# Optimization experiments

Hardware: AMD Instinct MI355X
Metric: run time of the kernel (lower is better)

## Reference

```python
import jax, jax.numpy as jnp
import numpy as np

HIDDEN = 256
HEADS = 8
HEAD_DIM = HIDDEN // HEADS
NUM_RBF = 32
CUTOFF = 8.0
K_PTS = 4096   # total points (32 molecules x 128)
N_ATOMS = 2048 # total atoms  (32 molecules x 64)
B_MOL = 32


def setup_inputs() -> dict:
    key = jax.random.key(0)
    ks = jax.random.split(key, 12)
    s = 0.02
    return {
        "h_point": jax.random.normal(ks[0], (K_PTS, HIDDEN), jnp.float32),
        "h_atom": jax.random.normal(ks[1], (N_ATOMS, HIDDEN), jnp.float32),
        "pos_point": jax.random.uniform(ks[2], (K_PTS, 3), jnp.float32) * 10.0,
        "pos_atom": jax.random.uniform(ks[3], (N_ATOMS, 3), jnp.float32) * 10.0,
        "Wq": jax.random.normal(ks[4], (HIDDEN, HIDDEN), jnp.float32) * s,
        "bq": jnp.zeros((HIDDEN,), jnp.float32),
        "Wk": jax.random.normal(ks[5], (HIDDEN, HIDDEN), jnp.float32) * s,
        "bk": jnp.zeros((HIDDEN,), jnp.float32),
        "Wv": jax.random.normal(ks[6], (HIDDEN, HIDDEN), jnp.float32) * s,
        "bv": jnp.zeros((HIDDEN,), jnp.float32),
        "Wo": jax.random.normal(ks[7], (HIDDEN, HIDDEN), jnp.float32) * s,
        "bo": jnp.zeros((HIDDEN,), jnp.float32),
        "W_rbf": jax.random.normal(ks[8], (NUM_RBF, HEADS), jnp.float32) * 0.1,
        "b_rbf": jnp.zeros((HEADS,), jnp.float32),
        "centers": jnp.linspace(0.0, CUTOFF, NUM_RBF, dtype=jnp.float32),
        "gamma": jnp.ones((HIDDEN,), jnp.float32),
        "beta": jnp.zeros((HIDDEN,), jnp.float32),
        "point_batch": jnp.repeat(jnp.arange(B_MOL), K_PTS // B_MOL),
        "atom_batch": jnp.repeat(jnp.arange(B_MOL), N_ATOMS // B_MOL),
    }


def reference(h_point, h_atom, pos_point, pos_atom,
              Wq, bq, Wk, bk, Wv, bv, Wo, bo,
              W_rbf, b_rbf, centers, gamma, beta,
              point_batch, atom_batch):
    H, D = HEADS, HEAD_DIM
    Kp = h_point.shape[0]
    Na = h_atom.shape[0]
    scale = D ** -0.5
    width = (CUTOFF / NUM_RBF) ** 2

    q = (h_point @ Wq + bq).reshape(Kp, H, D)
    k = (h_atom @ Wk + bk).reshape(Na, H, D)
    v = (h_atom @ Wv + bv).reshape(Na, H, D)

    # pairwise distances [Kp, Na]
    d2 = jnp.sum((pos_point[:, None, :] - pos_atom[None, :, :]) ** 2, axis=-1)
    dist = jnp.sqrt(jnp.maximum(d2, 0.0))

    # RBF distance bias -> [H, Kp, Na]
    rbf = jnp.exp(-((dist[..., None] - centers) ** 2) / width)  # [Kp, Na, NUM_RBF]
    bias = (rbf @ W_rbf + b_rbf).transpose(2, 0, 1)

    scores = jnp.einsum('khd,nhd->hkn', q, k) * scale + bias
    # ragged structure: point j only attends to atoms in the same molecule
    mask = point_batch[:, None] == atom_batch[None, :]  # [Kp, Na]
    scores = jnp.where(mask[None], scores, -1e30)
    attn = jax.nn.softmax(scores, axis=-1)

    agg = jnp.einsum('hkn,nhd->khd', attn, v).reshape(Kp, H * D)
    agg = agg @ Wo + bo

    x = h_point + agg
    mean = jnp.mean(x, axis=-1, keepdims=True)
    var = jnp.mean((x - mean) ** 2, axis=-1, keepdims=True)
    return (x - mean) * jax.lax.rsqrt(var + 1e-5) * gamma + beta
```

## Files before the change

kernel.cpp:

```cpp
#include <hip/hip_runtime.h>
#include <hip/hip_bf16.h>

#define HIDDEN 256
#define HEADS 8
#define HEAD_DIM 32
#define NUM_RBF 32
#define K_PTS 4096
#define N_ATOMS 2048
#define B_MOL 32
#define ATOMS_PER_MOL (N_ATOMS / B_MOL)

typedef __attribute__((ext_vector_type(8))) short bf16x8;
typedef __attribute__((ext_vector_type(4))) float f32x4;

__global__ __launch_bounds__(256) void prep2_kernel(
    const float* __restrict__ hp, const float* __restrict__ ha,
    const float* __restrict__ Wq, const float* __restrict__ Wk,
    const float* __restrict__ Wv, const float* __restrict__ Wo,
    __hip_bfloat16* __restrict__ hpb, __hip_bfloat16* __restrict__ hab,
    __hip_bfloat16* __restrict__ WqT, __hip_bfloat16* __restrict__ WkT,
    __hip_bfloat16* __restrict__ WvT, __hip_bfloat16* __restrict__ WoT) {
    const int b = blockIdx.x, tid = threadIdx.x;
    if (b < 768) {
        const bool isP = (b < 512);
        const float* __restrict__ src = isP ? hp : ha;
        __hip_bfloat16* __restrict__ dst = isP ? hpb : hab;
        const int e8 = ((isP ? b : b - 512) * 256 + tid);
        const float4* s4 = (const float4*)src;
        const float4 lo = s4[e8 * 2 + 0];
        const float4 hi = s4[e8 * 2 + 1];
        __hip_bfloat16 t[8];
        t[0] = __float2bfloat16(lo.x); t[1] = __float2bfloat16(lo.y);
        t[2] = __float2bfloat16(lo.z); t[3] = __float2bfloat16(lo.w);
        t[4] = __float2bfloat16(hi.x); t[5] = __float2bfloat16(hi.y);
        t[6] = __float2bfloat16(hi.z); t[7] = __float2bfloat16(hi.w);
        *(uint4*)(dst + (size_t)e8 * 8) = *(const uint4*)t;
        return;
    }
    __shared__ float tile[32][33];
    const int t = b - 768;
    const int matId = t >> 6, tileId = t & 63;
    const int tr = (tileId >> 3) * 32, tc = (tileId & 7) * 32;
    const float* __restrict__ Ws = (matId == 0) ? Wq : (matId == 1) ? Wk : (matId == 2) ? Wv : Wo;
    __hip_bfloat16* __restrict__ Wd = (matId == 0) ? WqT : (matId == 1) ? WkT : (matId == 2) ? WvT : WoT;

    const int r = tid >> 3, cq = (tid & 7) * 4;
    const float4 in = *(const float4*)&Ws[(size_t)(tr + r) * HIDDEN + tc + cq];
    tile[r][cq + 0] = in.x; tile[r][cq + 1] = in.y;
    tile[r][cq + 2] = in.z; tile[r][cq + 3] = in.w;
    __syncthreads();
    __hip_bfloat16 o[4];
    o[0] = __float2bfloat16(tile[cq + 0][r]);
    o[1] = __float2bfloat16(tile[cq + 1][r]);
    o[2] = __float2bfloat16(tile[cq + 2][r]);
    o[3] = __float2bfloat16(tile[cq + 3][r]);
    *(uint2*)(Wd + (size_t)(tc + r) * HIDDEN + tr + cq) = *(const uint2*)o;
}

__global__ __launch_bounds__(256) void qkv_kernel(
    const __hip_bfloat16* __restrict__ hpb, const __hip_bfloat16* __restrict__ hab,
    const __hip_bfloat16* __restrict__ WqT, const float* __restrict__ bq, float* __restrict__ q_ws,
    const __hip_bfloat16* __restrict__ WkT, const float* __restrict__ bk, float* __restrict__ k_ws,
    const __hip_bfloat16* __restrict__ WvT, const float* __restrict__ bv, float* __restrict__ v_ws) {
    const bool isQ = (blockIdx.x < 256);
    const __hip_bfloat16* __restrict__ A = isQ ? hpb : hab;
    const __hip_bfloat16* __restrict__ W0T = isQ ? WqT : WkT;
    const float* __restrict__ b0 = isQ ? bq : bk;
    float* __restrict__ C0 = isQ ? q_ws : k_ws;
    const int r0 = (isQ ? blockIdx.x : blockIdx.x - 256) * 16;

    const int wave = threadIdx.x >> 6, lane = threadIdx.x & 63;
    const int c0 = wave * 64;
    const int lrow = lane & 15, kgrp = lane >> 4;

    bf16x8 af[8];
    const short* Arow = (const short*)A + (size_t)(r0 + lrow) * HIDDEN + kgrp * 8;
#pragma unroll
    for (int ks = 0; ks < 8; ++ks)
        af[ks] = *(const bf16x8*)(Arow + ks * 32);

    f32x4 acc0[4], acc1[4];
#pragma unroll
    for (int cc = 0; cc < 4; ++cc) {
        acc0[cc] = (f32x4){0.f, 0.f, 0.f, 0.f};
        acc1[cc] = (f32x4){0.f, 0.f, 0.f, 0.f};
    }

#pragma unroll
    for (int cc = 0; cc < 4; ++cc) {
        const short* W0r = (const short*)W0T + (size_t)(c0 + cc * 16 + lrow) * HIDDEN + kgrp * 8;
#pragma unroll
        for (int ks = 0; ks < 8; ++ks)
            acc0[cc] = __builtin_amdgcn_mfma_f32_16x16x32_bf16(
                af[ks], *(const bf16x8*)(W0r + ks * 32), acc0[cc], 0, 0, 0);
        if (!isQ) {
            const short* W1r = (const short*)WvT + (size_t)(c0 + cc * 16 + lrow) * HIDDEN + kgrp * 8;
#pragma unroll
            for (int ks = 0; ks < 8; ++ks)
                acc1[cc] = __builtin_amdgcn_mfma_f32_16x16x32_bf16(
                    af[ks], *(const bf16x8*)(W1r + ks * 32), acc1[cc], 0, 0, 0);
        }
    }

    const int colb = lane & 15;
    const int rowb = (lane >> 4) * 4;
#pragma unroll
    for (int cc = 0; cc < 4; ++cc) {
        const int cgl = c0 + cc * 16 + colb;
        const float bias0 = b0[cgl];
#pragma unroll
        for (int rg = 0; rg < 4; ++rg)
            C0[(size_t)(r0 + rowb + rg) * HIDDEN + cgl] = acc0[cc][rg] + bias0;
        if (!isQ) {
            const float bias1 = bv[cgl];
#pragma unroll
            for (int rg = 0; rg < 4; ++rg)
                v_ws[(size_t)(r0 + rowb + rg) * HIDDEN + cgl] = acc1[cc][rg] + bias1;
        }
    }
}

__global__ __launch_bounds__(256) void attn3_kernel(
    const float* __restrict__ q, const float* __restrict__ kmat,
    const float* __restrict__ vmat,
    const float* __restrict__ pos_point, const float* __restrict__ pos_atom,
    const float* __restrict__ W_rbf, const float* __restrict__ b_rbf,
    const float* __restrict__ centers,
    const int* __restrict__ point_batch, const int* __restrict__ atom_batch,
    __hip_bfloat16* __restrict__ aggb) {
    __shared__ float q_lds[8][HIDDEN];
    __shared__ float wrbf_lds[NUM_RBF][HEADS];
    __shared__ float cent_lds[NUM_RBF];
    __shared__ float brbf_lds[HEADS];
    __shared__ float w_lds[4][2][HEADS][72];

    const int tid = threadIdx.x, wave = tid >> 6, lane = tid & 63;
    const int j0 = blockIdx.x * 8;

    {
        const float4* s4 = (const float4*)(q + (size_t)j0 * HIDDEN);
        float4* d4 = (float4*)&q_lds[0][0];
        d4[tid] = s4[tid];
        d4[tid + 256] = s4[tid + 256];
    }
    if (tid < NUM_RBF * HEADS) ((float*)wrbf_lds)[tid] = W_rbf[tid];
    if (tid < NUM_RBF) cent_lds[tid] = centers[tid];
    if (tid < HEADS) brbf_lds[tid] = b_rbf[tid];
    __syncthreads();

    const int jA = j0 + wave * 2, jB = jA + 1;
    const int m = point_batch[jA];
    const int n = m * ATOMS_PER_MOL + lane;
    const bool valid = (atom_batch[n] == m);

    const float ax = pos_atom[n * 3 + 0], ay = pos_atom[n * 3 + 1], az = pos_atom[n * 3 + 2];
    const float dxA = pos_point[jA * 3 + 0] - ax;
    const float dyA = pos_point[jA * 3 + 1] - ay;
    const float dzA = pos_point[jA * 3 + 2] - az;
    const float dxB = pos_point[jB * 3 + 0] - ax;
    const float dyB = pos_point[jB * 3 + 1] - ay;
    const float dzB = pos_point[jB * 3 + 2] - az;
    const float distA = sqrtf(fmaxf(dxA * dxA + dyA * dyA + dzA * dzA, 0.0f));
    const float distB = sqrtf(fmaxf(dxB * dxB + dyB * dyB + dzB * dzB, 0.0f));

    float biasA[HEADS], biasB[HEADS];
#pragma unroll
    for (int h = 0; h < HEADS; ++h) { biasA[h] = brbf_lds[h]; biasB[h] = brbf_lds[h]; }
#pragma unroll
    for (int r = 0; r < NUM_RBF; ++r) {
        const float c = cent_lds[r];
        const float ddA = distA - c, ddB = distB - c;
        const float eA = __expf(-16.0f * ddA * ddA);
        const float eB = __expf(-16.0f * ddB * ddB);
#pragma unroll
        for (int h = 0; h < HEADS; ++h) {
            const float wr = wrbf_lds[r][h];
            biasA[h] += eA * wr;
            biasB[h] += eB * wr;
        }
    }

    const float scale = 0.17677669529663687f;
    const float* krow = kmat + (size_t)n * HIDDEN;

#pragma unroll
    for (int h = 0; h < HEADS; ++h) {
        const float4* k4 = (const float4*)(krow + h * HEAD_DIM);
        const float4* qA4 = (const float4*)(&q_lds[wave * 2 + 0][h * HEAD_DIM]);
        const float4* qB4 = (const float4*)(&q_lds[wave * 2 + 1][h * HEAD_DIM]);
        float dotA = 0.f, dotB = 0.f;
#pragma unroll
        for (int i = 0; i < HEAD_DIM / 4; ++i) {
            const float4 kv = k4[i];
            const float4 qa = qA4[i];
            const float4 qb = qB4[i];
            dotA += kv.x * qa.x + kv.y * qa.y + kv.z * qa.z + kv.w * qa.w;
            dotB += kv.x * qb.x + kv.y * qb.y + kv.z * qb.z + kv.w * qb.w;
        }
        float sA = valid ? (dotA * scale + biasA[h]) : -1e30f;
        float sB = valid ? (dotB * scale + biasB[h]) : -1e30f;

        float mA = sA, mB = sB;
#pragma unroll
        for (int off = 32; off > 0; off >>= 1) {
            mA = fmaxf(mA, __shfl_xor(mA, off));
            mB = fmaxf(mB, __shfl_xor(mB, off));
        }
        const float eA = __expf(sA - mA);
        const float eB = __expf(sB - mB);
        float ssA = eA, ssB = eB;
#pragma unroll
        for (int off = 32; off > 0; off >>= 1) {
            ssA += __shfl_xor(ssA, off);
            ssB += __shfl_xor(ssB, off);
        }
        w_lds[wave][0][h][lane] = eA / ssA;
        w_lds[wave][1][h][lane] = eB / ssB;
    }

    const int c4 = lane * 4;
    const int hh = lane >> 3;
    const float* wA = &w_lds[wave][0][hh][0];
    const float* wB = &w_lds[wave][1][hh][0];
    const float* vbase = vmat + (size_t)(m * ATOMS_PER_MOL) * HIDDEN + c4;
    float4 accA = {0.f, 0.f, 0.f, 0.f};
    float4 accB = {0.f, 0.f, 0.f, 0.f};
#pragma unroll
    for (int a4 = 0; a4 < ATOMS_PER_MOL / 4; ++a4) {
        const float4 wa = *(const float4*)&wA[a4 * 4];
        const float4 wb = *(const float4*)&wB[a4 * 4];
        const float4 v0 = *(const float4*)(vbase + (size_t)(a4 * 4 + 0) * HIDDEN);
        const float4 v1 = *(const float4*)(vbase + (size_t)(a4 * 4 + 1) * HIDDEN);
        const float4 v2 = *(const float4*)(vbase + (size_t)(a4 * 4 + 2) * HIDDEN);
        const float4 v3 = *(const float4*)(vbase + (size_t)(a4 * 4 + 3) * HIDDEN);
        accA.x += wa.x * v0.x + wa.y * v1.x + wa.z * v2.x + wa.w * v3.x;
        accA.y += wa.x * v0.y + wa.y * v1.y + wa.z * v2.y + wa.w * v3.y;
        accA.z += wa.x * v0.z + wa.y * v1.z + wa.z * v2.z + wa.w * v3.z;
        accA.w += wa.x * v0.w + wa.y * v1.w + wa.z * v2.w + wa.w * v3.w;
        accB.x += wb.x * v0.x + wb.y * v1.x + wb.z * v2.x + wb.w * v3.x;
        accB.y += wb.x * v0.y + wb.y * v1.y + wb.z * v2.y + wb.w * v3.y;
        accB.z += wb.x * v0.z + wb.y * v1.z + wb.z * v2.z + wb.w * v3.z;
        accB.w += wb.x * v0.w + wb.y * v1.w + wb.z * v2.w + wb.w * v3.w;
    }
    {
        __hip_bfloat16 oA[4], oB[4];
        oA[0] = __float2bfloat16(accA.x); oA[1] = __float2bfloat16(accA.y);
        oA[2] = __float2bfloat16(accA.z); oA[3] = __float2bfloat16(accA.w);
        oB[0] = __float2bfloat16(accB.x); oB[1] = __float2bfloat16(accB.y);
        oB[2] = __float2bfloat16(accB.z); oB[3] = __float2bfloat16(accB.w);
        *(uint2*)(aggb + (size_t)jA * HIDDEN + c4) = *(const uint2*)oA;
        *(uint2*)(aggb + (size_t)jB * HIDDEN + c4) = *(const uint2*)oB;
    }
}

__global__ __launch_bounds__(256) void gemm_o_ln_kernel(
    const __hip_bfloat16* __restrict__ A,
    const __hip_bfloat16* __restrict__ WoT, const float* __restrict__ bo,
    const float* __restrict__ h_point,
    const float* __restrict__ gamma, const float* __restrict__ beta,
    float* __restrict__ out) {
    __shared__ float x_lds[16][HIDDEN + 1];
    __shared__ float red_s[16][4];
    __shared__ float red_q[16][4];

    const int r0 = blockIdx.x * 16;
    const int wave = threadIdx.x >> 6, lane = threadIdx.x & 63;
    const int c0 = wave * 64;
    const int lrow = lane & 15, kgrp = lane >> 4;

    bf16x8 af[8];
    const short* Arow = (const short*)A + (size_t)(r0 + lrow) * HIDDEN + kgrp * 8;
#pragma unroll
    for (int ks = 0; ks < 8; ++ks)
        af[ks] = *(const bf16x8*)(Arow + ks * 32);

    f32x4 acc[4];
#pragma unroll
    for (int cc = 0; cc < 4; ++cc) acc[cc] = (f32x4){0.f, 0.f, 0.f, 0.f};

#pragma unroll
    for (int cc = 0; cc < 4; ++cc) {
        const short* Wr = (const short*)WoT + (size_t)(c0 + cc * 16 + lrow) * HIDDEN + kgrp * 8;
#pragma unroll
        for (int ks = 0; ks < 8; ++ks)
            acc[cc] = __builtin_amdgcn_mfma_f32_16x16x32_bf16(
                af[ks], *(const bf16x8*)(Wr + ks * 32), acc[cc], 0, 0, 0);
    }

    const int colb = lane & 15;
    const int rowb = (lane >> 4) * 4;
#pragma unroll
    for (int cc = 0; cc < 4; ++cc) {
        const int cgl = c0 + cc * 16 + colb;
        const float bias = bo[cgl];
#pragma unroll
        for (int rg = 0; rg < 4; ++rg) {
            const int rl = rowb + rg;
            x_lds[rl][cgl] = acc[cc][rg] + bias + h_point[(size_t)(r0 + rl) * HIDDEN + cgl];
        }
    }
    __syncthreads();

    const int c = threadIdx.x;
    const int ln = c & 63, wv = c >> 6;
    float xv[16];
#pragma unroll
    for (int r = 0; r < 16; ++r) {
        xv[r] = x_lds[r][c];
        float s = xv[r], qq = xv[r] * xv[r];
#pragma unroll
        for (int off = 32; off > 0; off >>= 1) {
            s += __shfl_xor(s, off);
            qq += __shfl_xor(qq, off);
        }
        if (ln == 0) { red_s[r][wv] = s; red_q[r][wv] = qq; }
    }
    __syncthreads();

    const float gc = gamma[c], bc = beta[c];
#pragma unroll
    for (int r = 0; r < 16; ++r) {
        const float mean = (red_s[r][0] + red_s[r][1] + red_s[r][2] + red_s[r][3]) * (1.0f / HIDDEN);
        const float ex2  = (red_q[r][0] + red_q[r][1] + red_q[r][2] + red_q[r][3]) * (1.0f / HIDDEN);
        const float var = ex2 - mean * mean;
        out[(size_t)(r0 + r) * HIDDEN + c] = (xv[r] - mean) * rsqrtf(var + 1e-5f) * gc + bc;
    }
}

extern "C" void kernel_launch(void* const* d_in, const int* in_sizes, int n_in,
                              void* d_out, int out_size, void* d_ws, size_t ws_size,
                              hipStream_t stream) {
    const float* h_point   = (const float*)d_in[0];
    const float* h_atom    = (const float*)d_in[1];
    const float* pos_point = (const float*)d_in[2];
    const float* pos_atom  = (const float*)d_in[3];
    const float* Wq        = (const float*)d_in[4];
    const float* bq        = (const float*)d_in[5];
    const float* Wk        = (const float*)d_in[6];
    const float* bk        = (const float*)d_in[7];
    const float* Wv        = (const float*)d_in[8];
    const float* bv        = (const float*)d_in[9];
    const float* Wo        = (const float*)d_in[10];
    const float* bo        = (const float*)d_in[11];
    const float* W_rbf     = (const float*)d_in[12];
    const float* b_rbf     = (const float*)d_in[13];
    const float* centers   = (const float*)d_in[14];
    const float* gamma     = (const float*)d_in[15];
    const float* beta      = (const float*)d_in[16];
    const int*   point_batch = (const int*)d_in[17];
    const int*   atom_batch  = (const int*)d_in[18];
    float* out = (float*)d_out;

    float* q_ws = (float*)d_ws;
    float* k_ws = q_ws + (size_t)K_PTS * HIDDEN;
    float* v_ws = k_ws + (size_t)N_ATOMS * HIDDEN;
    __hip_bfloat16* hp_b = (__hip_bfloat16*)(v_ws + (size_t)N_ATOMS * HIDDEN);
    __hip_bfloat16* ha_b = hp_b + (size_t)K_PTS * HIDDEN;
    __hip_bfloat16* WqT = ha_b + (size_t)N_ATOMS * HIDDEN;
    __hip_bfloat16* WkT = WqT + HIDDEN * HIDDEN;
    __hip_bfloat16* WvT = WkT + HIDDEN * HIDDEN;
    __hip_bfloat16* WoT = WvT + HIDDEN * HIDDEN;
    __hip_bfloat16* agg_b = hp_b;

    prep2_kernel<<<1024, 256, 0, stream>>>(h_point, h_atom, Wq, Wk, Wv, Wo,
                                           hp_b, ha_b, WqT, WkT, WvT, WoT);

    qkv_kernel<<<384, 256, 0, stream>>>(hp_b, ha_b,
                                        WqT, bq, q_ws,
                                        WkT, bk, k_ws,
                                        WvT, bv, v_ws);

    attn3_kernel<<<K_PTS / 8, 256, 0, stream>>>(q_ws, k_ws, v_ws, pos_point, pos_atom,
                                                W_rbf, b_rbf, centers,
                                                point_batch, atom_batch, agg_b);

    gemm_o_ln_kernel<<<K_PTS / 16, 256, 0, stream>>>(agg_b, WoT, bo, h_point,
                                                     gamma, beta, out);
}
```

Before: 147.1 us.

## Fuse activation bf16 conversion into QKV GEMM and O-proj+LayerNorm into attention

The bf16 conversion of h_point/h_atom moves out of the prep kernel and into the QKV GEMM's A-fragment loads, which removes one round trip of the activations through global memory. The output projection and LayerNorm are fused into the attention kernel: the aggregated rows stay in LDS as bf16 and feed MFMA directly, so the separate gemm_o_ln launch and the agg round trip go away. The cost is that the fused GEMM now handles 8 rows per block, padded to 16, so half the MFMA rows do wasted work, and each block reloads the WoT matrix.

```diff
diff --git a/kernel.cpp b/kernel.cpp
--- a/kernel.cpp
+++ b/kernel.cpp
@@ -13,32 +13,13 @@
 typedef __attribute__((ext_vector_type(8))) short bf16x8;
 typedef __attribute__((ext_vector_type(4))) float f32x4;
 
-__global__ __launch_bounds__(256) void prep2_kernel(
-    const float* __restrict__ hp, const float* __restrict__ ha,
+__global__ __launch_bounds__(256) void prepW_kernel(
     const float* __restrict__ Wq, const float* __restrict__ Wk,
     const float* __restrict__ Wv, const float* __restrict__ Wo,
-    __hip_bfloat16* __restrict__ hpb, __hip_bfloat16* __restrict__ hab,
     __hip_bfloat16* __restrict__ WqT, __hip_bfloat16* __restrict__ WkT,
     __hip_bfloat16* __restrict__ WvT, __hip_bfloat16* __restrict__ WoT) {
-    const int b = blockIdx.x, tid = threadIdx.x;
-    if (b < 768) {
-        const bool isP = (b < 512);
-        const float* __restrict__ src = isP ? hp : ha;
-        __hip_bfloat16* __restrict__ dst = isP ? hpb : hab;
-        const int e8 = ((isP ? b : b - 512) * 256 + tid);
-        const float4* s4 = (const float4*)src;
-        const float4 lo = s4[e8 * 2 + 0];
-        const float4 hi = s4[e8 * 2 + 1];
-        __hip_bfloat16 t[8];
-        t[0] = __float2bfloat16(lo.x); t[1] = __float2bfloat16(lo.y);
-        t[2] = __float2bfloat16(lo.z); t[3] = __float2bfloat16(lo.w);
-        t[4] = __float2bfloat16(hi.x); t[5] = __float2bfloat16(hi.y);
-        t[6] = __float2bfloat16(hi.z); t[7] = __float2bfloat16(hi.w);
-        *(uint4*)(dst + (size_t)e8 * 8) = *(const uint4*)t;
-        return;
-    }
     __shared__ float tile[32][33];
-    const int t = b - 768;
+    const int t = blockIdx.x, tid = threadIdx.x;
     const int matId = t >> 6, tileId = t & 63;
     const int tr = (tileId >> 3) * 32, tc = (tileId & 7) * 32;
     const float* __restrict__ Ws = (matId == 0) ? Wq : (matId == 1) ? Wk : (matId == 2) ? Wv : Wo;
@@ -57,13 +38,24 @@
     *(uint2*)(Wd + (size_t)(tc + r) * HIDDEN + tr + cq) = *(const uint2*)o;
 }
 
-__global__ __launch_bounds__(256) void qkv_kernel(
-    const __hip_bfloat16* __restrict__ hpb, const __hip_bfloat16* __restrict__ hab,
+__device__ __forceinline__ bf16x8 cvt8(const float* p) {
+    const float4 lo = *(const float4*)p;
+    const float4 hi = *(const float4*)(p + 4);
+    __hip_bfloat16 t[8];
+    t[0] = __float2bfloat16(lo.x); t[1] = __float2bfloat16(lo.y);
+    t[2] = __float2bfloat16(lo.z); t[3] = __float2bfloat16(lo.w);
+    t[4] = __float2bfloat16(hi.x); t[5] = __float2bfloat16(hi.y);
+    t[6] = __float2bfloat16(hi.z); t[7] = __float2bfloat16(hi.w);
+    return *(const bf16x8*)t;
+}
+
+__global__ __launch_bounds__(256) void qkv2_kernel(
+    const float* __restrict__ hp, const float* __restrict__ ha,
     const __hip_bfloat16* __restrict__ WqT, const float* __restrict__ bq, float* __restrict__ q_ws,
     const __hip_bfloat16* __restrict__ WkT, const float* __restrict__ bk, float* __restrict__ k_ws,
     const __hip_bfloat16* __restrict__ WvT, const float* __restrict__ bv, float* __restrict__ v_ws) {
     const bool isQ = (blockIdx.x < 256);
-    const __hip_bfloat16* __restrict__ A = isQ ? hpb : hab;
+    const float* __restrict__ A = isQ ? hp : ha;
     const __hip_bfloat16* __restrict__ W0T = isQ ? WqT : WkT;
     const float* __restrict__ b0 = isQ ? bq : bk;
     float* __restrict__ C0 = isQ ? q_ws : k_ws;
@@ -74,10 +66,10 @@
     const int lrow = lane & 15, kgrp = lane >> 4;
 
     bf16x8 af[8];
-    const short* Arow = (const short*)A + (size_t)(r0 + lrow) * HIDDEN + kgrp * 8;
+    const float* Arow = A + (size_t)(r0 + lrow) * HIDDEN + kgrp * 8;
 #pragma unroll
     for (int ks = 0; ks < 8; ++ks)
-        af[ks] = *(const bf16x8*)(Arow + ks * 32);
+        af[ks] = cvt8(Arow + ks * 32);
 
     f32x4 acc0[4], acc1[4];
 #pragma unroll
@@ -120,19 +112,29 @@
     }
 }
 
-__global__ __launch_bounds__(256) void attn3_kernel(
+#define AGG_PAD (HIDDEN + 16)
+#define X_PAD (HIDDEN + 4)
+
+__global__ __launch_bounds__(256) void attn_oln_kernel(
     const float* __restrict__ q, const float* __restrict__ kmat,
     const float* __restrict__ vmat,
     const float* __restrict__ pos_point, const float* __restrict__ pos_atom,
     const float* __restrict__ W_rbf, const float* __restrict__ b_rbf,
     const float* __restrict__ centers,
     const int* __restrict__ point_batch, const int* __restrict__ atom_batch,
-    __hip_bfloat16* __restrict__ aggb) {
+    const __hip_bfloat16* __restrict__ WoT, const float* __restrict__ bo,
+    const float* __restrict__ h_point,
+    const float* __restrict__ gamma, const float* __restrict__ beta,
+    float* __restrict__ out) {
     __shared__ float q_lds[8][HIDDEN];
     __shared__ float wrbf_lds[NUM_RBF][HEADS];
     __shared__ float cent_lds[NUM_RBF];
     __shared__ float brbf_lds[HEADS];
     __shared__ float w_lds[4][2][HEADS][72];
+    __shared__ __hip_bfloat16 agg_lds[8][AGG_PAD];
+    __shared__ float x_lds[8][X_PAD];
+    __shared__ float red_s[8][4];
+    __shared__ float red_q[8][4];
 
     const int tid = threadIdx.x, wave = tid >> 6, lane = tid & 63;
     const int j0 = blockIdx.x * 8;
@@ -220,64 +222,50 @@
 
     const int c4 = lane * 4;
     const int hh = lane >> 3;
-    const float* wA = &w_lds[wave][0][hh][0];
-    const float* wB = &w_lds[wave][1][hh][0];
-    const float* vbase = vmat + (size_t)(m * ATOMS_PER_MOL) * HIDDEN + c4;
-    float4 accA = {0.f, 0.f, 0.f, 0.f};
-    float4 accB = {0.f, 0.f, 0.f, 0.f};
-#pragma unroll
-    for (int a4 = 0; a4 < ATOMS_PER_MOL / 4; ++a4) {
-        const float4 wa = *(const float4*)&wA[a4 * 4];
-        const float4 wb = *(const float4*)&wB[a4 * 4];
-        const float4 v0 = *(const float4*)(vbase + (size_t)(a4 * 4 + 0) * HIDDEN);
-        const float4 v1 = *(const float4*)(vbase + (size_t)(a4 * 4 + 1) * HIDDEN);
-        const float4 v2 = *(const float4*)(vbase + (size_t)(a4 * 4 + 2) * HIDDEN);
-        const float4 v3 = *(const float4*)(vbase + (size_t)(a4 * 4 + 3) * HIDDEN);
-        accA.x += wa.x * v0.x + wa.y * v1.x + wa.z * v2.x + wa.w * v3.x;
-        accA.y += wa.x * v0.y + wa.y * v1.y + wa.z * v2.y + wa.w * v3.y;
-        accA.z += wa.x * v0.z + wa.y * v1.z + wa.z * v2.z + wa.w * v3.z;
-        accA.w += wa.x * v0.w + wa.y * v1.w + wa.z * v2.w + wa.w * v3.w;
-        accB.x += wb.x * v0.x + wb.y * v1.x + wb.z * v2.x + wb.w * v3.x;
-        accB.y += wb.x * v0.y + wb.y * v1.y + wb.z * v2.y + wb.w * v3.y;
-        accB.z += wb.x * v0.z + wb.y * v1.z + wb.z * v2.z + wb.w * v3.z;
-        accB.w += wb.x * v0.w + wb.y * v1.w + wb.z * v2.w + wb.w * v3.w;
-    }
     {
+        const float* wA = &w_lds[wave][0][hh][0];
+        const float* wB = &w_lds[wave][1][hh][0];
+        const float* vbase = vmat + (size_t)(m * ATOMS_PER_MOL) * HIDDEN + c4;
+        float4 accA = {0.f, 0.f, 0.f, 0.f};
+        float4 accB = {0.f, 0.f, 0.f, 0.f};
+#pragma unroll
+        for (int a4 = 0; a4 < ATOMS_PER_MOL / 4; ++a4) {
+            const float4 wa = *(const float4*)&wA[a4 * 4];
+            const float4 wb = *(const float4*)&wB[a4 * 4];
+            const float4 v0 = *(const float4*)(vbase + (size_t)(a4 * 4 + 0) * HIDDEN);
+            const float4 v1 = *(const float4*)(vbase + (size_t)(a4 * 4 + 1) * HIDDEN);
+            const float4 v2 = *(const float4*)(vbase + (size_t)(a4 * 4 + 2) * HIDDEN);
+            const float4 v3 = *(const float4*)(vbase + (size_t)(a4 * 4 + 3) * HIDDEN);
+            accA.x += wa.x * v0.x + wa.y * v1.x + wa.z * v2.x + wa.w * v3.x;
+            accA.y += wa.x * v0.y + wa.y * v1.y + wa.z * v2.y + wa.w * v3.y;
+            accA.z += wa.x * v0.z + wa.y * v1.z + wa.z * v2.z + wa.w * v3.z;
+            accA.w += wa.x * v0.w + wa.y * v1.w + wa.z * v2.w + wa.w * v3.w;
+            accB.x += wb.x * v0.x + wb.y * v1.x + wb.z * v2.x + wb.w * v3.x;
+            accB.y += wb.x * v0.y + wb.y * v1.y + wb.z * v2.y + wb.w * v3.y;
+            accB.z += wb.x * v0.z + wb.y * v1.z + wb.z * v2.z + wb.w * v3.z;
+            accB.w += wb.x * v0.w + wb.y * v1.w + wb.z * v2.w + wb.w * v3.w;
+        }
         __hip_bfloat16 oA[4], oB[4];
         oA[0] = __float2bfloat16(accA.x); oA[1] = __float2bfloat16(accA.y);
         oA[2] = __float2bfloat16(accA.z); oA[3] = __float2bfloat16(accA.w);
         oB[0] = __float2bfloat16(accB.x); oB[1] = __float2bfloat16(accB.y);
         oB[2] = __float2bfloat16(accB.z); oB[3] = __float2bfloat16(accB.w);
-        *(uint2*)(aggb + (size_t)jA * HIDDEN + c4) = *(const uint2*)oA;
-        *(uint2*)(aggb + (size_t)jB * HIDDEN + c4) = *(const uint2*)oB;
-    }
-}
-
-__global__ __launch_bounds__(256) void gemm_o_ln_kernel(
-    const __hip_bfloat16* __restrict__ A,
-    const __hip_bfloat16* __restrict__ WoT, const float* __restrict__ bo,
-    const float* __restrict__ h_point,
-    const float* __restrict__ gamma, const float* __restrict__ beta,
-    float* __restrict__ out) {
-    __shared__ float x_lds[16][HIDDEN + 1];
-    __shared__ float red_s[16][4];
-    __shared__ float red_q[16][4];
-
-    const int r0 = blockIdx.x * 16;
-    const int wave = threadIdx.x >> 6, lane = threadIdx.x & 63;
+        *(uint2*)(&agg_lds[wave * 2 + 0][c4]) = *(const uint2*)oA;
+        *(uint2*)(&agg_lds[wave * 2 + 1][c4]) = *(const uint2*)oB;
+    }
+    __syncthreads();
+
     const int c0 = wave * 64;
     const int lrow = lane & 15, kgrp = lane >> 4;
-
     bf16x8 af[8];
-    const short* Arow = (const short*)A + (size_t)(r0 + lrow) * HIDDEN + kgrp * 8;
+    const bf16x8 zf = {0, 0, 0, 0, 0, 0, 0, 0};
 #pragma unroll
     for (int ks = 0; ks < 8; ++ks)
-        af[ks] = *(const bf16x8*)(Arow + ks * 32);
+        af[ks] = (lrow < 8) ? *(const bf16x8*)(&agg_lds[lrow & 7][kgrp * 8 + ks * 32]) : zf;
 
     f32x4 acc[4];
 #pragma unroll
     for (int cc = 0; cc < 4; ++cc) acc[cc] = (f32x4){0.f, 0.f, 0.f, 0.f};
-
 #pragma unroll
     for (int cc = 0; cc < 4; ++cc) {
         const short* Wr = (const short*)WoT + (size_t)(c0 + cc * 16 + lrow) * HIDDEN + kgrp * 8;
@@ -296,16 +284,17 @@
 #pragma unroll
         for (int rg = 0; rg < 4; ++rg) {
             const int rl = rowb + rg;
-            x_lds[rl][cgl] = acc[cc][rg] + bias + h_point[(size_t)(r0 + rl) * HIDDEN + cgl];
-        }
-    }
-    __syncthreads();
-
-    const int c = threadIdx.x;
+            if (rl < 8)
+                x_lds[rl][cgl] = acc[cc][rg] + bias + h_point[(size_t)(j0 + rl) * HIDDEN + cgl];
+        }
+    }
+    __syncthreads();
+
+    const int c = tid;
     const int ln = c & 63, wv = c >> 6;
-    float xv[16];
-#pragma unroll
-    for (int r = 0; r < 16; ++r) {
+    float xv[8];
+#pragma unroll
+    for (int r = 0; r < 8; ++r) {
         xv[r] = x_lds[r][c];
         float s = xv[r], qq = xv[r] * xv[r];
 #pragma unroll
@@ -319,11 +308,11 @@
 
     const float gc = gamma[c], bc = beta[c];
 #pragma unroll
-    for (int r = 0; r < 16; ++r) {
+    for (int r = 0; r < 8; ++r) {
         const float mean = (red_s[r][0] + red_s[r][1] + red_s[r][2] + red_s[r][3]) * (1.0f / HIDDEN);
         const float ex2  = (red_q[r][0] + red_q[r][1] + red_q[r][2] + red_q[r][3]) * (1.0f / HIDDEN);
         const float var = ex2 - mean * mean;
-        out[(size_t)(r0 + r) * HIDDEN + c] = (xv[r] - mean) * rsqrtf(var + 1e-5f) * gc + bc;
+        out[(size_t)(j0 + r) * HIDDEN + c] = (xv[r] - mean) * rsqrtf(var + 1e-5f) * gc + bc;
     }
 }
 
@@ -354,26 +343,22 @@
     float* q_ws = (float*)d_ws;
     float* k_ws = q_ws + (size_t)K_PTS * HIDDEN;
     float* v_ws = k_ws + (size_t)N_ATOMS * HIDDEN;
-    __hip_bfloat16* hp_b = (__hip_bfloat16*)(v_ws + (size_t)N_ATOMS * HIDDEN);
-    __hip_bfloat16* ha_b = hp_b + (size_t)K_PTS * HIDDEN;
-    __hip_bfloat16* WqT = ha_b + (size_t)N_ATOMS * HIDDEN;
+    __hip_bfloat16* WqT = (__hip_bfloat16*)(v_ws + (size_t)N_ATOMS * HIDDEN);
     __hip_bfloat16* WkT = WqT + HIDDEN * HIDDEN;
     __hip_bfloat16* WvT = WkT + HIDDEN * HIDDEN;
     __hip_bfloat16* WoT = WvT + HIDDEN * HIDDEN;
-    __hip_bfloat16* agg_b = hp_b;
-
-    prep2_kernel<<<1024, 256, 0, stream>>>(h_point, h_atom, Wq, Wk, Wv, Wo,
-                                           hp_b, ha_b, WqT, WkT, WvT, WoT);
-
-    qkv_kernel<<<384, 256, 0, stream>>>(hp_b, ha_b,
-                                        WqT, bq, q_ws,
-                                        WkT, bk, k_ws,
-                                        WvT, bv, v_ws);
-
-    attn3_kernel<<<K_PTS / 8, 256, 0, stream>>>(q_ws, k_ws, v_ws, pos_point, pos_atom,
-                                                W_rbf, b_rbf, centers,
-                                                point_batch, atom_batch, agg_b);
-
-    gemm_o_ln_kernel<<<K_PTS / 16, 256, 0, stream>>>(agg_b, WoT, bo, h_point,
-                                                     gamma, beta, out);
-}
+
+    prepW_kernel<<<256, 256, 0, stream>>>(Wq, Wk, Wv, Wo, WqT, WkT, WvT, WoT);
+
+    qkv2_kernel<<<384, 256, 0, stream>>>(h_point, h_atom,
+                                         WqT, bq, q_ws,
+                                         WkT, bk, k_ws,
+                                         WvT, bv, v_ws);
+
+    attn_oln_kernel<<<K_PTS / 8, 256, 0, stream>>>(q_ws, k_ws, v_ws,
+                                                   pos_point, pos_atom,
+                                                   W_rbf, b_rbf, centers,
+                                                   point_batch, atom_batch,
+                                                   WoT, bo, h_point, gamma, beta,
+                                                   out);
+}
```

Result: no change. 146.7 us (-0.2%).
